# Kernel optimization log

Measured on AMD Instinct MI355X. Metric: run time of the kernel, lower is better.

Reference implementation:

```python
import jax, jax.numpy as jnp
import numpy as np

XLIM = 6.0    # params.max_rdf_dist
DR = 0.05     # params.dr
N_BINS = int(XLIM / DR)  # 120


def setup_inputs() -> dict:
    key = jax.random.key(0)
    k1, k2, k3 = jax.random.split(key, 3)
    T, R, N = 100, 8, 83  # frames, replicas, LiPS atoms
    L = 10.2              # LiPS lattice constant (Angstrom)
    stacked_radii = jax.random.uniform(k1, (T, R, N, 3), dtype=jnp.float32) * L
    # near-cubic LiPS cell with a tiny random skew (non-degenerate lattice)
    cell = jnp.eye(3, dtype=jnp.float32) * L + 0.1 * jax.random.uniform(k2, (3, 3), dtype=jnp.float32)
    gt_rdf = jax.random.uniform(k3, (N_BINS,), dtype=jnp.float32)
    bins = jnp.linspace(1e-6, XLIM, N_BINS + 1).astype(jnp.float32)
    return {"stacked_radii": stacked_radii, "cell": cell, "gt_rdf": gt_rdf, "bins": bins}


def _histogram(d, bins):
    # np.histogram semantics: values outside [bins[0], bins[-1]] dropped,
    # right edge inclusive in the last bin. Zeros (self-distances) fall
    # below bins[0]=1e-6, matching the original's d != 0 filter.
    nb = bins.shape[0] - 1
    idx = jnp.clip(jnp.searchsorted(bins, d, side='right') - 1, 0, nb - 1)
    w = ((d >= bins[0]) & (d <= bins[-1])).astype(jnp.float32)
    return jax.ops.segment_sum(w, idx, num_segments=nb)


def _min_image_dist(x, shifts):
    # x: [T, N, 3]; shifts: [27, 3]. Loop over the 27 fixed shifts to avoid
    # materializing the [T, N, N, 27, 3] tensor the torch code builds.
    diff = x[:, :, None, :] - x[:, None, :, :]            # [T, N, N, 3]
    d2 = jnp.sum((diff - shifts[0]) ** 2, axis=-1)        # [T, N, N]
    for i in range(1, shifts.shape[0]):
        d2 = jnp.minimum(d2, jnp.sum((diff - shifts[i]) ** 2, axis=-1))
    return jnp.sqrt(d2)


def reference(stacked_radii, cell, gt_rdf, bins):
    T, R, N, _ = stacked_radii.shape
    pos = np.arange(-1, 2)  # num_cells = 1 -> 27 periodic images
    combos = jnp.asarray(
        np.stack(np.meshgrid(pos, pos, pos, indexing='xy'), axis=-1).reshape(-1, 3),
        dtype=stacked_radii.dtype)                        # [27, 3]
    shifts = combos @ cell                                # [27, 3]
    volume = jnp.abs(jnp.dot(jnp.cross(cell[0], cell[1]), cell[2]))
    rho = (T * N * N) / volume  # data_shape counted BEFORE zero-filter, as in original
    Z = rho * (4.0 / 3.0) * jnp.pi * (bins[1:] ** 3 - bins[:-1] ** 3)  # [n_bins]

    def rdf_one(x):  # x: [T, N, 3] -> [n_bins]
        d = _min_image_dist(x, shifts)
        return _histogram(d.reshape(-1), bins) / Z

    rdfs = jax.vmap(rdf_one, in_axes=1)(stacked_radii)    # [R, n_bins]
    maes = XLIM * jnp.mean(jnp.abs(rdfs - gt_rdf), axis=-1, keepdims=True)  # [R, 1]
    return rdfs, maes
```

## Files before the change

kernel.cpp:

```cpp
#include <hip/hip_runtime.h>

#define T_FRAMES 100
#define R_REP    8
#define N_ATOMS  83
#define N_BINS   120
#define NWORDS   60
#define NPAIRS   (N_ATOMS * (N_ATOMS - 1) / 2)
#define BLK      256
#define PPT      7
#define HALF0    1702
#define SLOTS    (2 * T_FRAMES)

__device__ __forceinline__ int rowstart(int i) {
    return (i * (165 - i)) >> 1;
}

__global__ __launch_bounds__(BLK, 4) void rdf_hist_kernel(
        const float* __restrict__ radii,
        const float* __restrict__ cell,
        const float* __restrict__ bins,
        unsigned int* __restrict__ partial)
{
#pragma clang fp contract(off)
    __shared__ float sx[N_ATOMS], sy[N_ATOMS], sz[N_ATOMS];
    __shared__ float sfx[N_ATOMS], sfy[N_ATOMS], sfz[N_ATOMS];
    __shared__ float sbins[N_BINS + 1];
    __shared__ unsigned int shist[N_BINS];

    const int tid  = threadIdx.x;
    const int blk  = blockIdx.x;
    const int fr   = blk >> 1;
    const int half = blk & 1;
    const int t = fr / R_REP;
    const int r = fr % R_REP;
    const int pstart = half ? HALF0 : 0;
    const int pcount = half ? (NPAIRS - HALF0) : HALF0;

    float cc[3][3];
#pragma unroll
    for (int c = 0; c < 3; ++c)
#pragma unroll
        for (int d = 0; d < 3; ++d) cc[c][d] = cell[c * 3 + d];
    float rn[3];
#pragma unroll
    for (int c = 0; c < 3; ++c)
        rn[c] = 1.0f / (cc[c][0] * cc[c][0] + cc[c][1] * cc[c][1] + cc[c][2] * cc[c][2]);

    for (int i = tid; i < N_ATOMS; i += BLK) {
        const float* p = radii + (((size_t)t * R_REP + r) * N_ATOMS + i) * 3;
        const float x = p[0], y = p[1], z = p[2];
        sx[i] = x; sy[i] = y; sz[i] = z;
        sfx[i] = (x * cc[0][0] + y * cc[0][1] + z * cc[0][2]) * rn[0];
        sfy[i] = (x * cc[1][0] + y * cc[1][1] + z * cc[1][2]) * rn[1];
        sfz[i] = (x * cc[2][0] + y * cc[2][1] + z * cc[2][2]) * rn[2];
    }
    for (int i = tid; i <= N_BINS; i += BLK) sbins[i] = bins[i];
    for (int i = tid; i < N_BINS; i += BLK) shist[i] = 0u;
    __syncthreads();

    float dx[PPT], dy[PPT], dz[PPT], fx[PPT], fy[PPT], fz[PPT];
#pragma unroll
    for (int s = 0; s < PPT; ++s) {
        const int l = tid + s * BLK;
        const int p = (l < pcount) ? (pstart + l) : 0;
        int i = (int)((165.0f - sqrtf((float)(27225 - 8 * p))) * 0.5f);
        if (i < 0) i = 0;
        if (i > N_ATOMS - 2) i = N_ATOMS - 2;
        while (rowstart(i + 1) <= p) ++i;
        while (rowstart(i) > p) --i;
        const int j = p - rowstart(i) + i + 1;
        dx[s] = sx[i] - sx[j];
        dy[s] = sy[i] - sy[j];
        dz[s] = sz[i] - sz[j];
        fx[s] = sfx[i] - sfx[j];
        fy[s] = sfy[i] - sfy[j];
        fz[s] = sfz[i] - sfz[j];
    }

    float d2m[PPT];
#pragma unroll
    for (int s = 0; s < PPT; ++s) {
        const float Dx = dx[s], Dy = dy[s], Dz = dz[s];
        int axi = (int)floorf(fx[s]); axi = axi < -1 ? -1 : (axi > 0 ? 0 : axi);
        int ayi = (int)floorf(fy[s]); ayi = ayi < -1 ? -1 : (ayi > 0 ? 0 : ayi);
        int azi = (int)floorf(fz[s]); azi = azi < -1 ? -1 : (azi > 0 ? 0 : azi);
        const float na0 = (float)axi, na1 = na0 + 1.0f;
        const float nb0 = (float)ayi, nb1 = nb0 + 1.0f;
        const float nc0 = (float)azi, nc1 = nc0 + 1.0f;

        float An[2][3], Bn[2][3], Cn[2][3];
#pragma unroll
        for (int d = 0; d < 3; ++d) {
            An[0][d] = na0 * cc[0][d]; An[1][d] = na1 * cc[0][d];
            Bn[0][d] = nb0 * cc[1][d]; Bn[1][d] = nb1 * cc[1][d];
            Cn[0][d] = nc0 * cc[2][d]; Cn[1][d] = nc1 * cc[2][d];
        }
        float m = 3.4e38f;
#pragma unroll
        for (int ia = 0; ia < 2; ++ia) {
#pragma unroll
            for (int ib = 0; ib < 2; ++ib) {
                const float m0 = An[ia][0] + Bn[ib][0];
                const float m1 = An[ia][1] + Bn[ib][1];
                const float m2 = An[ia][2] + Bn[ib][2];
#pragma unroll
                for (int ic = 0; ic < 2; ++ic) {
                    const float t0 = Dx - (m0 + Cn[ic][0]);
                    const float t1 = Dy - (m1 + Cn[ic][1]);
                    const float t2 = Dz - (m2 + Cn[ic][2]);
                    const float d2 = (t0 * t0 + t1 * t1) + t2 * t2;
                    m = fminf(m, d2);
                }
            }
        }
        d2m[s] = m;
    }

    const float blo = sbins[0];
    const float inv_step = (float)N_BINS / (6.0f - blo);
#pragma unroll
    for (int s = 0; s < PPT; ++s) {
        const int l = tid + s * BLK;
        if (l >= pcount) continue;
        if (d2m[s] > 36.0f) continue;
        const float d = sqrtf(d2m[s]);
        if (d >= blo) {
            int idx = (int)((d - blo) * inv_step);
            if (idx > N_BINS - 1) idx = N_BINS - 1;
            if (idx < 0) idx = 0;
            while (idx > 0 && d < sbins[idx]) --idx;
            while (idx < N_BINS - 1 && d >= sbins[idx + 1]) ++idx;
            atomicAdd(&shist[idx], 2u);
        }
    }
    __syncthreads();

    if (tid < NWORDS) {
        const unsigned int w = shist[2 * tid] | (shist[2 * tid + 1] << 16);
        partial[((size_t)(r * SLOTS + t * 2 + half)) * NWORDS + tid] = w;
    }
}

__global__ __launch_bounds__(256) void finalize_kernel(
        const unsigned int* __restrict__ partial,
        const float* __restrict__ cell,
        const float* __restrict__ bins,
        const float* __restrict__ gt,
        float* __restrict__ out)
{
    __shared__ unsigned int slo[4][NWORDS], shi[4][NWORDS];
    __shared__ float sdiff[N_BINS];
    const int r = blockIdx.x;
    const int tid = threadIdx.x;
    const int h = tid >> 6;
    const int c = tid & 63;

    if (c < NWORDS) {
        const unsigned int* base = partial
            + (size_t)r * SLOTS * NWORDS + (size_t)h * 50 * NWORDS + c;
        unsigned int lo = 0, hi = 0;
#pragma unroll 10
        for (int f = 0; f < 50; ++f) {
            const unsigned int w = base[(size_t)f * NWORDS];
            lo += w & 0xFFFFu;
            hi += w >> 16;
        }
        slo[h][c] = lo;
        shi[h][c] = hi;
    }
    __syncthreads();

    const float c0x = cell[0], c0y = cell[1], c0z = cell[2];
    const float c1x = cell[3], c1y = cell[4], c1z = cell[5];
    const float c2x = cell[6], c2y = cell[7], c2z = cell[8];
    const float crx = c0y * c1z - c0z * c1y;
    const float cry = c0z * c1x - c0x * c1z;
    const float crz = c0x * c1y - c0y * c1x;
    const float vol = fabsf(crx * c2x + cry * c2y + crz * c2z);
    const float rho = (float)(T_FRAMES * N_ATOMS * N_ATOMS) / vol;
    const float coef = (rho * 1.33333337f) * 3.14159274f;

    if (tid < N_BINS) {
        const int w = tid >> 1;
        unsigned int tot = 0;
        if (tid & 1) tot = shi[0][w] + shi[1][w] + shi[2][w] + shi[3][w];
        else         tot = slo[0][w] + slo[1][w] + slo[2][w] + slo[3][w];
        const float b1 = bins[tid], b2 = bins[tid + 1];
        const float Z = coef * (b2 * b2 * b2 - b1 * b1 * b1);
        const float v = (float)tot / Z;
        out[r * N_BINS + tid] = v;
        sdiff[tid] = fabsf(v - gt[tid]);
    }
    __syncthreads();

    if (tid < 64) {
        float s = sdiff[tid] + ((tid < N_BINS - 64) ? sdiff[tid + 64] : 0.0f);
#pragma unroll
        for (int off = 32; off; off >>= 1) s += __shfl_down(s, off, 64);
        if (tid == 0)
            out[R_REP * N_BINS + r] = 6.0f * (s * (1.0f / (float)N_BINS));
    }
}

extern "C" void kernel_launch(void* const* d_in, const int* in_sizes, int n_in,
                              void* d_out, int out_size, void* d_ws, size_t ws_size,
                              hipStream_t stream) {
    const float* radii = (const float*)d_in[0];
    const float* cell  = (const float*)d_in[1];
    const float* gt    = (const float*)d_in[2];
    const float* bins  = (const float*)d_in[3];
    float* out = (float*)d_out;
    unsigned int* part = (unsigned int*)d_ws;

    hipLaunchKernelGGL(rdf_hist_kernel, dim3(2 * T_FRAMES * R_REP), dim3(BLK), 0, stream,
                       radii, cell, bins, part);
    hipLaunchKernelGGL(finalize_kernel, dim3(R_REP), dim3(256), 0, stream,
                       part, cell, bins, gt, out);
}
```

Baseline: 27.57 us.

## Use one 512-thread block per frame with float4 shared atom data

Each (frame, replica) is now handled by a single 512-thread block instead of two 256-thread blocks that split the pair list, which halves the block count and the partial histogram slots. Atom positions and fractional coordinates are stored as float4 in shared memory so each atom needs one vector load, and the image offsets are computed during the pair gather. This removes the duplicated per-block setup (atom loads, bins, histogram init) and the extra partial writes, at the cost of fewer blocks (800) for the GPU to spread across CUs and one fewer occupancy hint.

```diff
diff --git a/kernel.cpp b/kernel.cpp
--- a/kernel.cpp
+++ b/kernel.cpp
@@ -6,35 +6,30 @@
 #define N_BINS   120
 #define NWORDS   60
 #define NPAIRS   (N_ATOMS * (N_ATOMS - 1) / 2)
-#define BLK      256
+#define BLK      512
 #define PPT      7
-#define HALF0    1702
-#define SLOTS    (2 * T_FRAMES)
+#define SLOTS    T_FRAMES
 
 __device__ __forceinline__ int rowstart(int i) {
     return (i * (165 - i)) >> 1;
 }
 
-__global__ __launch_bounds__(BLK, 4) void rdf_hist_kernel(
+__global__ __launch_bounds__(BLK) void rdf_hist_kernel(
         const float* __restrict__ radii,
         const float* __restrict__ cell,
         const float* __restrict__ bins,
         unsigned int* __restrict__ partial)
 {
 #pragma clang fp contract(off)
-    __shared__ float sx[N_ATOMS], sy[N_ATOMS], sz[N_ATOMS];
-    __shared__ float sfx[N_ATOMS], sfy[N_ATOMS], sfz[N_ATOMS];
+    __shared__ float4 spos[N_ATOMS];
+    __shared__ float4 sfrac[N_ATOMS];
     __shared__ float sbins[N_BINS + 1];
     __shared__ unsigned int shist[N_BINS];
 
-    const int tid  = threadIdx.x;
-    const int blk  = blockIdx.x;
-    const int fr   = blk >> 1;
-    const int half = blk & 1;
-    const int t = fr / R_REP;
-    const int r = fr % R_REP;
-    const int pstart = half ? HALF0 : 0;
-    const int pcount = half ? (NPAIRS - HALF0) : HALF0;
+    const int tid = threadIdx.x;
+    const int blk = blockIdx.x;
+    const int t = blk / R_REP;
+    const int r = blk % R_REP;
 
     float cc[3][3];
 #pragma unroll
@@ -46,47 +41,48 @@
     for (int c = 0; c < 3; ++c)
         rn[c] = 1.0f / (cc[c][0] * cc[c][0] + cc[c][1] * cc[c][1] + cc[c][2] * cc[c][2]);
 
-    for (int i = tid; i < N_ATOMS; i += BLK) {
-        const float* p = radii + (((size_t)t * R_REP + r) * N_ATOMS + i) * 3;
+    if (tid < N_ATOMS) {
+        const float* p = radii + (((size_t)t * R_REP + r) * N_ATOMS + tid) * 3;
         const float x = p[0], y = p[1], z = p[2];
-        sx[i] = x; sy[i] = y; sz[i] = z;
-        sfx[i] = (x * cc[0][0] + y * cc[0][1] + z * cc[0][2]) * rn[0];
-        sfy[i] = (x * cc[1][0] + y * cc[1][1] + z * cc[1][2]) * rn[1];
-        sfz[i] = (x * cc[2][0] + y * cc[2][1] + z * cc[2][2]) * rn[2];
-    }
-    for (int i = tid; i <= N_BINS; i += BLK) sbins[i] = bins[i];
-    for (int i = tid; i < N_BINS; i += BLK) shist[i] = 0u;
-    __syncthreads();
-
-    float dx[PPT], dy[PPT], dz[PPT], fx[PPT], fy[PPT], fz[PPT];
+        spos[tid] = make_float4(x, y, z, 0.f);
+        sfrac[tid] = make_float4(
+            (x * cc[0][0] + y * cc[0][1] + z * cc[0][2]) * rn[0],
+            (x * cc[1][0] + y * cc[1][1] + z * cc[1][2]) * rn[1],
+            (x * cc[2][0] + y * cc[2][1] + z * cc[2][2]) * rn[2], 0.f);
+    }
+    if (tid <= N_BINS) sbins[tid] = bins[tid];
+    if (tid < N_BINS) shist[tid] = 0u;
+    __syncthreads();
+
+    float dx[PPT], dy[PPT], dz[PPT], na[PPT], nb[PPT], nc[PPT];
 #pragma unroll
     for (int s = 0; s < PPT; ++s) {
         const int l = tid + s * BLK;
-        const int p = (l < pcount) ? (pstart + l) : 0;
+        const int p = (l < NPAIRS) ? l : 0;
         int i = (int)((165.0f - sqrtf((float)(27225 - 8 * p))) * 0.5f);
         if (i < 0) i = 0;
         if (i > N_ATOMS - 2) i = N_ATOMS - 2;
         while (rowstart(i + 1) <= p) ++i;
         while (rowstart(i) > p) --i;
         const int j = p - rowstart(i) + i + 1;
-        dx[s] = sx[i] - sx[j];
-        dy[s] = sy[i] - sy[j];
-        dz[s] = sz[i] - sz[j];
-        fx[s] = sfx[i] - sfx[j];
-        fy[s] = sfy[i] - sfy[j];
-        fz[s] = sfz[i] - sfz[j];
+        const float4 pi = spos[i], pj = spos[j];
+        const float4 qi = sfrac[i], qj = sfrac[j];
+        dx[s] = pi.x - pj.x;
+        dy[s] = pi.y - pj.y;
+        dz[s] = pi.z - pj.z;
+        int axi = (int)floorf(qi.x - qj.x); axi = axi < -1 ? -1 : (axi > 0 ? 0 : axi);
+        int ayi = (int)floorf(qi.y - qj.y); ayi = ayi < -1 ? -1 : (ayi > 0 ? 0 : ayi);
+        int azi = (int)floorf(qi.z - qj.z); azi = azi < -1 ? -1 : (azi > 0 ? 0 : azi);
+        na[s] = (float)axi; nb[s] = (float)ayi; nc[s] = (float)azi;
     }
 
     float d2m[PPT];
 #pragma unroll
     for (int s = 0; s < PPT; ++s) {
         const float Dx = dx[s], Dy = dy[s], Dz = dz[s];
-        int axi = (int)floorf(fx[s]); axi = axi < -1 ? -1 : (axi > 0 ? 0 : axi);
-        int ayi = (int)floorf(fy[s]); ayi = ayi < -1 ? -1 : (ayi > 0 ? 0 : ayi);
-        int azi = (int)floorf(fz[s]); azi = azi < -1 ? -1 : (azi > 0 ? 0 : azi);
-        const float na0 = (float)axi, na1 = na0 + 1.0f;
-        const float nb0 = (float)ayi, nb1 = nb0 + 1.0f;
-        const float nc0 = (float)azi, nc1 = nc0 + 1.0f;
+        const float na0 = na[s], na1 = na0 + 1.0f;
+        const float nb0 = nb[s], nb1 = nb0 + 1.0f;
+        const float nc0 = nc[s], nc1 = nc0 + 1.0f;
 
         float An[2][3], Bn[2][3], Cn[2][3];
 #pragma unroll
@@ -121,7 +117,7 @@
 #pragma unroll
     for (int s = 0; s < PPT; ++s) {
         const int l = tid + s * BLK;
-        if (l >= pcount) continue;
+        if (l >= NPAIRS) continue;
         if (d2m[s] > 36.0f) continue;
         const float d = sqrtf(d2m[s]);
         if (d >= blo) {
@@ -137,7 +133,7 @@
 
     if (tid < NWORDS) {
         const unsigned int w = shist[2 * tid] | (shist[2 * tid + 1] << 16);
-        partial[((size_t)(r * SLOTS + t * 2 + half)) * NWORDS + tid] = w;
+        partial[((size_t)(r * SLOTS + t)) * NWORDS + tid] = w;
     }
 }
 
@@ -157,10 +153,10 @@
 
     if (c < NWORDS) {
         const unsigned int* base = partial
-            + (size_t)r * SLOTS * NWORDS + (size_t)h * 50 * NWORDS + c;
+            + (size_t)r * SLOTS * NWORDS + (size_t)h * 25 * NWORDS + c;
         unsigned int lo = 0, hi = 0;
-#pragma unroll 10
-        for (int f = 0; f < 50; ++f) {
+#pragma unroll 5
+        for (int f = 0; f < 25; ++f) {
             const unsigned int w = base[(size_t)f * NWORDS];
             lo += w & 0xFFFFu;
             hi += w >> 16;
@@ -212,7 +208,7 @@
     float* out = (float*)d_out;
     unsigned int* part = (unsigned int*)d_ws;
 
-    hipLaunchKernelGGL(rdf_hist_kernel, dim3(2 * T_FRAMES * R_REP), dim3(BLK), 0, stream,
+    hipLaunchKernelGGL(rdf_hist_kernel, dim3(T_FRAMES * R_REP), dim3(BLK), 0, stream,
                        radii, cell, bins, part);
     hipLaunchKernelGGL(finalize_kernel, dim3(R_REP), dim3(256), 0, stream,
                        part, cell, bins, gt, out);
```

New measurement: 27.81 us. No clear change (+0.9%).
